# Optimization experiments

Measured on AMD Instinct MI355X. Metric: run time of the kernel, lower is better.

## Reference

```python
import jax, jax.numpy as jnp
import numpy as np

B, S, D, H, DFF = 65536, 9, 20, 4, 512
DH = D // H  # 5
EPS = 1e-5


def _layernorm(x, g, b):
    m = jnp.mean(x, axis=-1, keepdims=True)
    v = jnp.mean(jnp.square(x - m), axis=-1, keepdims=True)
    return (x - m) * jax.lax.rsqrt(v + EPS) * g + b


def setup_inputs() -> dict:
    key = jax.random.key(0)
    ks = jax.random.split(key, 8)
    s = 1.0 / np.sqrt(D)
    inp = {
        "inputs": jax.random.normal(ks[0], (B, S, D), dtype=jnp.float32),
        "Wq": jax.random.uniform(ks[1], (D, D), jnp.float32, -s, s),
        "bq": jnp.zeros((D,), jnp.float32),
        "Wk": jax.random.uniform(ks[2], (D, D), jnp.float32, -s, s),
        "bk": jnp.zeros((D,), jnp.float32),
        "Wv": jax.random.uniform(ks[3], (D, D), jnp.float32, -s, s),
        "bv": jnp.zeros((D,), jnp.float32),
        "Wo": jax.random.uniform(ks[4], (D, D), jnp.float32, -s, s),
        "bo": jnp.zeros((D,), jnp.float32),
        "g1": jnp.ones((D,), jnp.float32),
        "b1": jnp.zeros((D,), jnp.float32),
        "W1": jax.random.uniform(ks[5], (D, DFF), jnp.float32, -s, s),
        "W2": jax.random.uniform(ks[6], (DFF, D), jnp.float32, -1.0 / np.sqrt(DFF), 1.0 / np.sqrt(DFF)),
        "g2": jnp.ones((D,), jnp.float32),
        "b2": jnp.zeros((D,), jnp.float32),
    }
    return inp


def reference(inputs, Wq, bq, Wk, bk, Wv, bv, Wo, bo, g1, b1, W1, W2, g2, b2):
    x = inputs  # [B,S,D]
    q = (x @ Wq + bq).reshape(B, S, H, DH).transpose(0, 2, 1, 3)  # [B,H,S,dh]
    k = (x @ Wk + bk).reshape(B, S, H, DH).transpose(0, 2, 1, 3)
    v = (x @ Wv + bv).reshape(B, S, H, DH).transpose(0, 2, 1, 3)
    a = jnp.einsum('bhqd,bhkd->bhqk', q, k) / 3.0  # hardcoded /3 in source
    attn = jax.nn.softmax(a, axis=-1)
    ctx = jnp.einsum('bhqk,bhkd->bhqd', attn, v)  # [B,H,S,dh]
    # faithful quirk: transpose(2,3) then reshape to [B,9,20]
    merged = ctx.transpose(0, 1, 3, 2).reshape(B, S, D)
    attn_out = merged @ Wo + bo
    y = _layernorm(attn_out + x, g1, b1)
    ff = jax.nn.relu(y @ W1) @ W2
    return _layernorm(y + ff, g2, b2)
```

## Files before the change

kernel.cpp:

```cpp
#include <hip/hip_runtime.h>
#include <hip/hip_bf16.h>
#include <hip/hip_fp16.h>

#define B_TOT 65536
#define S 9
#define D 20
#define DFF 512
#define EPS 1e-5f

typedef short bf16x8 __attribute__((ext_vector_type(8)));
typedef _Float16 f16x8 __attribute__((ext_vector_type(8)));
typedef float f32x4 __attribute__((ext_vector_type(4)));

#define SH_PQKV 0
#define SH_PWOA 2560
#define FL_BQKV2 1792
#define FL_BO4 1872
#define SH_PA1 3872
#define SH_PB2 20256
#define PREP_TOTAL (2560 + 1024 + 144 + 16384 + 16384)

__device__ __forceinline__ unsigned short f2bf(float f) {
  union { __hip_bfloat16 h; unsigned short u; } v;
  v.h = __float2bfloat16(f);
  return v.u;
}
__device__ __forceinline__ unsigned short f2h(float f) {
  union { _Float16 h; unsigned short u; } v;
  v.h = (_Float16)f;
  return v.u;
}
__device__ __forceinline__ float bf2f(unsigned short h) {
  union { unsigned u; float f; } v; v.u = ((unsigned)h) << 16; return v.f;
}
__device__ __forceinline__ unsigned cvt2(float a, float b) {
  union { __hip_bfloat162 h; unsigned u; } v;
  v.h = __float22bfloat162_rn(make_float2(a, b));
  return v.u;
}
__device__ __forceinline__ unsigned cvt2h(float a, float b) {
  union { __half2 h; unsigned u; } v;
  v.h = __float22half2_rn(make_float2(a, b));
  return v.u;
}
__device__ __forceinline__ void unpk(unsigned u, float& lo, float& hi) {
  union { unsigned v; float f; } a, b;
  a.v = u << 16; b.v = u & 0xffff0000u;
  lo = a.f; hi = b.f;
}
__device__ __forceinline__ void unpack20_u2(const char* p, float* o) {
  uint2 r0 = *(const uint2*)p, r1 = *(const uint2*)(p + 8), r2 = *(const uint2*)(p + 16);
  uint2 r3 = *(const uint2*)(p + 24), r4 = *(const uint2*)(p + 32);
  unpk(r0.x, o[0], o[1]); unpk(r0.y, o[2], o[3]);
  unpk(r1.x, o[4], o[5]); unpk(r1.y, o[6], o[7]);
  unpk(r2.x, o[8], o[9]); unpk(r2.y, o[10], o[11]);
  unpk(r3.x, o[12], o[13]); unpk(r3.y, o[14], o[15]);
  unpk(r4.x, o[16], o[17]); unpk(r4.y, o[18], o[19]);
}

union h2u { unsigned u; __half2 h; };

__global__ void prep_kernel(const float* __restrict__ Wq, const float* __restrict__ Wk,
                            const float* __restrict__ Wv, const float* __restrict__ Wo,
                            const float* __restrict__ W1, const float* __restrict__ W2,
                            const float* __restrict__ bq, const float* __restrict__ bk,
                            const float* __restrict__ bv, const float* __restrict__ bo,
                            float* __restrict__ wsf) {
  int stride = gridDim.x * blockDim.x;
  unsigned short* P = (unsigned short*)wsf;
  for (int i = blockIdx.x * blockDim.x + threadIdx.x; i < PREP_TOTAL; i += stride) {
    if (i < 2560) {
      int ct = i >> 9, rem = i & 511, l = rem >> 3, jj = rem & 7;
      int g = l >> 4, cl = l & 15;
      int jp = ct * 16 + cl, d = 8 * g + jj;
      unsigned short v = 0;
      if (d < 20 && jp < 72) {
        int mat = jp / 24, r24 = jp % 24;
        int h = r24 / 6, c6 = r24 % 6;
        if (c6 < 5) {
          const float* Wsrc = (mat == 0) ? Wq : (mat == 1) ? Wk : Wv;
          v = f2bf(Wsrc[d * 20 + 5 * h + c6]);
        }
      }
      P[SH_PQKV + i] = v;
    } else if (i < 3584) {
      int p = i - 2560;
      int ct = p >> 9, rem = p & 511, l = rem >> 3, jj = rem & 7;
      int g = l >> 4, cl = l & 15;
      int j = ct * 16 + cl, d = 8 * g + jj;
      P[SH_PWOA + p] = (d < 20 && j < 20) ? f2bf(Wo[d * 20 + j]) : (unsigned short)0;
    } else if (i < 3728) {
      int j = i - 3584;
      if (j < 80) {
        float v = 0.f;
        if (j < 72) {
          int mat = j / 24, r24 = j % 24;
          int h = r24 / 6, c6 = r24 % 6;
          if (c6 < 5) {
            const float* bsrc = (mat == 0) ? bq : (mat == 1) ? bk : bv;
            v = bsrc[5 * h + c6];
          }
        }
        wsf[FL_BQKV2 + j] = v;
      } else {
        int jb = j - 80;
        wsf[FL_BO4 + jb] = (jb < 20) ? bo[jb] : 0.f;
      }
    } else if (i < 3728 + 16384) {
      int j = i - 3728;
      int frag = j >> 9, rem = j & 511;
      int l = rem >> 3, jj = rem & 7;
      int p = frag & 1, q2 = (frag >> 1) & 3, ch = frag >> 3;
      int g2 = l >> 4, cl2 = l & 15;
      int k = 8 * g2 + jj;
      int f = ch * 128 + q2 * 32 + 8 * (cl2 >> 2) + 4 * p + (cl2 & 3);
      P[SH_PA1 + j] = (k < 20) ? f2bf(W1[k * DFF + f]) : (unsigned short)0;
    } else {
      int j = i - (3728 + 16384);
      int pair = j >> 9, rem = j & 511;
      int l = rem >> 3, jj = rem & 7;
      int g = l >> 4, cl = l & 15;
      int kk = pair >> 1, cc = pair & 1;
      int kg = kk * 32 + 8 * g + jj;
      int d = cc * 16 + cl;
      P[SH_PB2 + j] = (d < 20) ? f2h(W2[kg * 20 + d]) : (unsigned short)0;
    }
  }
}

#define SLAB_BYTES 13312
#define RA 0
#define RB 7168

#define FENCE() asm volatile("" ::: "memory")

__global__ __launch_bounds__(256, 2) void encoder_kernel(
    const float* __restrict__ X, const float* __restrict__ ws,
    const float* __restrict__ g1, const float* __restrict__ b1,
    const float* __restrict__ g2, const float* __restrict__ b2,
    float* __restrict__ Out) {
  __shared__ __align__(16) char smem[4 * SLAB_BYTES];

  const unsigned short* P16 = (const unsigned short*)ws;
  const unsigned short* PQKV = P16 + SH_PQKV;
  const unsigned short* PWOA = P16 + SH_PWOA;
  const float* BQKV2 = ws + FL_BQKV2;
  const float* BO4 = ws + FL_BO4;
  const unsigned short* PA1 = P16 + SH_PA1;
  const unsigned short* PB2 = P16 + SH_PB2;

  const int tid = threadIdx.x;
  const int wv = tid >> 6;
  const int lane = tid & 63;
  const int bl = lane / 9;
  const int s = lane - bl * 9;
  const long wb = (long)blockIdx.x * 4 + wv;
  const long bb = wb * 7 + bl;
  const bool active = (bl < 7) && (bb < B_TOT);

  char* slab = smem + wv * SLAB_BYTES;
  const int cl = lane & 15;
  const int g = lane >> 4;
  const f32x4 zero4 = {0.f, 0.f, 0.f, 0.f};

  float x[20];

  {
    if (active) {
      const float4* xr = (const float4*)(X + bb * (S * D) + s * D);
#pragma unroll
      for (int i = 0; i < 5; ++i) {
        float4 t = xr[i];
        x[4 * i + 0] = t.x; x[4 * i + 1] = t.y; x[4 * i + 2] = t.z; x[4 * i + 3] = t.w;
      }
    } else {
#pragma unroll
      for (int i = 0; i < 20; ++i) x[i] = 0.f;
    }
    unsigned u[10];
#pragma unroll
    for (int i = 0; i < 10; ++i) u[i] = cvt2(x[2 * i], x[2 * i + 1]);
    uint4* dst = (uint4*)(slab + RA + lane * 112);
    dst[0] = make_uint4(u[0], u[1], u[2], u[3]);
    dst[1] = make_uint4(u[4], u[5], u[6], u[7]);
    dst[2] = make_uint4(u[8], u[9], 0u, 0u);
    dst[3] = make_uint4(0u, 0u, 0u, 0u);
  }
  FENCE();

  bf16x8 xfB[4];
#pragma unroll
  for (int rtc = 0; rtc < 4; ++rtc)
    xfB[rtc] = *(const bf16x8*)(slab + RA + (rtc * 16 + cl) * 112 + g * 16);
  FENCE();

#pragma unroll
  for (int ct = 0; ct < 5; ++ct) {
    bf16x8 wf = *(const bf16x8*)(PQKV + (size_t)(ct * 64 + lane) * 8);
    float4 bq4 = *(const float4*)(BQKV2 + ct * 16 + 4 * g);
    const f32x4 cin = {bq4.x, bq4.y, bq4.z, bq4.w};
    const int qd = ct * 4 + g;
    const int mat = (qd >= 12) ? 2 : ((qd >= 6) ? 1 : 0);
    const int jq = qd - 6 * mat;
    const bool qv = qd < 18;
#pragma unroll
    for (int rtc = 0; rtc < 4; ++rtc) {
      f32x4 d = __builtin_amdgcn_mfma_f32_16x16x32_bf16(wf, xfB[rtc], cin, 0, 0, 0);
      if (qv) {
        const int row = rtc * 16 + cl;
        unsigned u0 = cvt2h(d[0], d[1]);
        unsigned u1 = cvt2h(d[2], d[3]);
        char* p = (mat == 0) ? (slab + RA + row * 112 + 64 + jq * 8)
                             : (slab + RB + row * 96 + ((mat == 2) ? 48 : 0) + jq * 8);
        *(uint2*)p = make_uint2(u0, u1);
      }
    }
  }
  FENCE();

  float ctx[20];
  if (active) {
    h2u q2[12];
    {
      const uint2* qp = (const uint2*)(slab + RA + lane * 112 + 64);
#pragma unroll
      for (int i = 0; i < 6; ++i) { uint2 t = qp[i]; q2[2 * i].u = t.x; q2[2 * i + 1].u = t.y; }
    }
    float sc[4][9];
#pragma unroll
    for (int t = 0; t < 9; ++t) {
      h2u k2[12];
      const uint2* kp = (const uint2*)(slab + RB + (bl * 9 + t) * 96);
#pragma unroll
      for (int i = 0; i < 6; ++i) { uint2 tt = kp[i]; k2[2 * i].u = tt.x; k2[2 * i + 1].u = tt.y; }
#pragma unroll
      for (int h = 0; h < 4; ++h) {
        __half2 a = __hmul2(q2[3 * h].h, k2[3 * h].h);
        a = __hfma2(q2[3 * h + 1].h, k2[3 * h + 1].h, a);
        a = __hfma2(q2[3 * h + 2].h, k2[3 * h + 2].h, a);
        sc[h][t] = __low2float(a) + __high2float(a);
      }
    }
    float inv4[4];
#pragma unroll
    for (int h = 0; h < 4; ++h) {
      float mx = sc[h][0];
#pragma unroll
      for (int t = 1; t < 9; ++t) mx = fmaxf(mx, sc[h][t]);
      float sum = 0.f;
#pragma unroll
      for (int t = 0; t < 9; ++t) {
        sc[h][t] = __expf((sc[h][t] - mx) * (1.0f / 3.0f));
        sum += sc[h][t];
      }
      inv4[h] = 1.0f / sum;
    }
    h2u ctx2[12];
#pragma unroll
    for (int i = 0; i < 12; ++i) ctx2[i].u = 0u;
#pragma unroll
    for (int t = 0; t < 9; ++t) {
      h2u v2[12];
      const uint2* vp = (const uint2*)(slab + RB + (bl * 9 + t) * 96 + 48);
#pragma unroll
      for (int i = 0; i < 6; ++i) { uint2 tt = vp[i]; v2[2 * i].u = tt.x; v2[2 * i + 1].u = tt.y; }
#pragma unroll
      for (int h = 0; h < 4; ++h) {
        __half2 p2 = __float2half2_rn(sc[h][t]);
#pragma unroll
        for (int p3 = 0; p3 < 3; ++p3)
          ctx2[3 * h + p3].h = __hfma2(p2, v2[3 * h + p3].h, ctx2[3 * h + p3].h);
      }
    }
#pragma unroll
    for (int h = 0; h < 4; ++h) {
      ctx[5 * h + 0] = __low2float(ctx2[3 * h + 0].h) * inv4[h];
      ctx[5 * h + 1] = __high2float(ctx2[3 * h + 0].h) * inv4[h];
      ctx[5 * h + 2] = __low2float(ctx2[3 * h + 1].h) * inv4[h];
      ctx[5 * h + 3] = __high2float(ctx2[3 * h + 1].h) * inv4[h];
      ctx[5 * h + 4] = __low2float(ctx2[3 * h + 2].h) * inv4[h];
    }
  }
  FENCE();

  if (active) {
    int m = s;
#pragma unroll
    for (int w = 0; w < 20; ++w) {
      int row = (m * 3277) >> 16;
      int col = m - 20 * row;
      *(unsigned short*)(slab + RB + (bl * 9 + row) * 80 + col * 2) = f2bf(ctx[w]);
      m += 9;
    }
  } else {
    *(uint4*)(slab + RB + lane * 80) = make_uint4(0u, 0u, 0u, 0u);
    *(uint4*)(slab + RB + lane * 80 + 16) = make_uint4(0u, 0u, 0u, 0u);
    *(uint2*)(slab + RB + lane * 80 + 32) = make_uint2(0u, 0u);
  }
  *(uint2*)(slab + RB + lane * 80 + 40) = make_uint2(0u, 0u);
  *(uint4*)(slab + RB + lane * 80 + 48) = make_uint4(0u, 0u, 0u, 0u);
  FENCE();

  bf16x8 mfB[4];
#pragma unroll
  for (int rtc = 0; rtc < 4; ++rtc)
    mfB[rtc] = *(const bf16x8*)(slab + RB + (rtc * 16 + cl) * 80 + g * 16);
  FENCE();
#pragma unroll
  for (int ct = 0; ct < 2; ++ct) {
    bf16x8 wof = *(const bf16x8*)(PWOA + (size_t)(ct * 64 + lane) * 8);
    float4 bo4 = *(const float4*)(BO4 + ct * 16 + 4 * g);
    const f32x4 cin = {bo4.x, bo4.y, bo4.z, bo4.w};
    const int qd = ct * 4 + g;
    const bool qv = qd < 5;
#pragma unroll
    for (int rtc = 0; rtc < 4; ++rtc) {
      f32x4 d = __builtin_amdgcn_mfma_f32_16x16x32_bf16(wof, mfB[rtc], cin, 0, 0, 0);
      if (qv) {
        const int row = rtc * 16 + cl;
        *(float4*)(slab + RB + row * 80 + qd * 16) = make_float4(d[0], d[1], d[2], d[3]);
      }
    }
  }
  FENCE();

  float y[20];
  if (active) {
    float ao[20];
    {
      const float4* ap = (const float4*)(slab + RB + lane * 80);
#pragma unroll
      for (int i = 0; i < 5; ++i) {
        float4 t = ap[i];
        ao[4 * i] = t.x; ao[4 * i + 1] = t.y; ao[4 * i + 2] = t.z; ao[4 * i + 3] = t.w;
      }
    }
    float z[20];
#pragma unroll
    for (int d = 0; d < 20; ++d) z[d] = ao[d] + x[d];
    float t0 = 0.f;
#pragma unroll
    for (int d = 0; d < 20; ++d) t0 += z[d];
    float mean = t0 * (1.0f / 20.0f);
    float var = 0.f;
#pragma unroll
    for (int d = 0; d < 20; ++d) { z[d] -= mean; var += z[d] * z[d]; }
    float rs = rsqrtf(var * (1.0f / 20.0f) + EPS);
#pragma unroll
    for (int d = 0; d < 20; ++d) y[d] = z[d] * rs * g1[d] + b1[d];
  } else {
#pragma unroll
    for (int d = 0; d < 20; ++d) y[d] = 0.f;
  }
  FENCE();

  {
    unsigned u[10];
#pragma unroll
    for (int i = 0; i < 10; ++i) u[i] = cvt2(y[2 * i], y[2 * i + 1]);
    uint4* dst = (uint4*)(slab + RA + lane * 112);
    dst[0] = make_uint4(u[0], u[1], u[2], u[3]);
    dst[1] = make_uint4(u[4], u[5], u[6], u[7]);
    *(uint2*)(slab + RA + lane * 112 + 32) = make_uint2(u[8], u[9]);
  }
  FENCE();

  bf16x8 ytf[4];
#pragma unroll
  for (int rt = 0; rt < 4; ++rt)
    ytf[rt] = *(const bf16x8*)(slab + RA + (rt * 16 + cl) * 112 + g * 16);

  f32x4 acc[4][2];
#pragma unroll
  for (int rt = 0; rt < 4; ++rt) { acc[rt][0] = zero4; acc[rt][1] = zero4; }

  for (int ch = 0; ch < 4; ++ch) {
#pragma unroll
    for (int q2 = 0; q2 < 4; ++q2) {
      const int fb = ch * 8 + q2 * 2;
      bf16x8 aw0 = *(const bf16x8*)(PA1 + (size_t)(fb * 64 + lane) * 8);
      bf16x8 aw1 = *(const bf16x8*)(PA1 + (size_t)((fb + 1) * 64 + lane) * 8);
      f16x8 bw0 = *(const f16x8*)(PB2 + (size_t)(fb * 64 + lane) * 8);
      f16x8 bw1 = *(const f16x8*)(PB2 + (size_t)((fb + 1) * 64 + lane) * 8);
#pragma unroll
      for (int rt = 0; rt < 4; ++rt) {
        f32x4 d0 = __builtin_amdgcn_mfma_f32_16x16x32_bf16(aw0, ytf[rt], zero4, 0, 0, 0);
        f32x4 d1 = __builtin_amdgcn_mfma_f32_16x16x32_bf16(aw1, ytf[rt], zero4, 0, 0, 0);
        union { f16x8 v; unsigned uu[4]; } af;
        af.uu[0] = cvt2h(fmaxf(d0[0], 0.f), fmaxf(d0[1], 0.f));
        af.uu[1] = cvt2h(fmaxf(d0[2], 0.f), fmaxf(d0[3], 0.f));
        af.uu[2] = cvt2h(fmaxf(d1[0], 0.f), fmaxf(d1[1], 0.f));
        af.uu[3] = cvt2h(fmaxf(d1[2], 0.f), fmaxf(d1[3], 0.f));
        acc[rt][0] = __builtin_amdgcn_mfma_f32_16x16x32_f16(af.v, bw0, acc[rt][0], 0, 0, 0);
        acc[rt][1] = __builtin_amdgcn_mfma_f32_16x16x32_f16(af.v, bw1, acc[rt][1], 0, 0, 0);
      }
    }
  }

#pragma unroll
  for (int rt = 0; rt < 4; ++rt) {
#pragma unroll
    for (int r = 0; r < 4; ++r) {
      const int rrow = rt * 16 + 4 * g + r;
      *(float*)(slab + RB + rrow * 88 + cl * 4) = acc[rt][0][r];
      if (cl < 4) *(float*)(slab + RB + rrow * 88 + 64 + cl * 4) = acc[rt][1][r];
    }
  }
  FENCE();

  if (active) {
    float z[20];
    {
      const char* fp = slab + RB + lane * 88;
#pragma unroll
      for (int i = 0; i < 10; ++i) {
        float2 t = *(const float2*)(fp + 8 * i);
        z[2 * i] = t.x; z[2 * i + 1] = t.y;
      }
    }
    float yr[20];
    unpack20_u2(slab + RA + lane * 112, yr);
    float t0 = 0.f;
#pragma unroll
    for (int d = 0; d < 20; ++d) { z[d] += yr[d]; t0 += z[d]; }
    float mean = t0 * (1.0f / 20.0f);
    float var = 0.f;
#pragma unroll
    for (int d = 0; d < 20; ++d) { z[d] -= mean; var += z[d] * z[d]; }
    float rs = rsqrtf(var * (1.0f / 20.0f) + EPS);
    float o[20];
#pragma unroll
    for (int d = 0; d < 20; ++d) o[d] = z[d] * rs * g2[d] + b2[d];
    float4* op = (float4*)(Out + (wb * 63 + lane) * 20);
#pragma unroll
    for (int i = 0; i < 5; ++i)
      op[i] = make_float4(o[4 * i], o[4 * i + 1], o[4 * i + 2], o[4 * i + 3]);
  }
}

extern "C" void kernel_launch(void* const* d_in, const int* in_sizes, int n_in,
                              void* d_out, int out_size, void* d_ws, size_t ws_size,
                              hipStream_t stream) {
  const float* X  = (const float*)d_in[0];
  const float* Wq = (const float*)d_in[1];
  const float* bq = (const float*)d_in[2];
  const float* Wk = (const float*)d_in[3];
  const float* bk = (const float*)d_in[4];
  const float* Wv = (const float*)d_in[5];
  const float* bv = (const float*)d_in[6];
  const float* Wo = (const float*)d_in[7];
  const float* bo = (const float*)d_in[8];
  const float* g1 = (const float*)d_in[9];
  const float* b1 = (const float*)d_in[10];
  const float* W1 = (const float*)d_in[11];
  const float* W2 = (const float*)d_in[12];
  const float* g2 = (const float*)d_in[13];
  const float* b2 = (const float*)d_in[14];
  float* Out = (float*)d_out;
  float* ws = (float*)d_ws;

  prep_kernel<<<144, 256, 0, stream>>>(Wq, Wk, Wv, Wo, W1, W2, bq, bk, bv, bo, ws);

  int nblocks = (B_TOT + 27) / 28;
  encoder_kernel<<<nblocks, 256, 0, stream>>>(X, ws, g1, b1, g2, b2, Out);
}
```

Baseline: 85.27 us.

## Pack QKV projection densely, shrink LDS slabs, and use packed f16 ReLU

```diff
diff --git a/kernel.cpp b/kernel.cpp
--- a/kernel.cpp
+++ b/kernel.cpp
@@ -13,12 +13,12 @@
 typedef float f32x4 __attribute__((ext_vector_type(4)));
 
 #define SH_PQKV 0
-#define SH_PWOA 2560
-#define FL_BQKV2 1792
-#define FL_BO4 1872
-#define SH_PA1 3872
-#define SH_PB2 20256
-#define PREP_TOTAL (2560 + 1024 + 144 + 16384 + 16384)
+#define SH_PWOA 2048
+#define FL_BQKV 1536
+#define FL_BO4 1600
+#define SH_PA1 3328
+#define SH_PB2 19712
+#define PREP_TOTAL (2048 + 1024 + 128 + 16384 + 16384)
 
 __device__ __forceinline__ unsigned short f2bf(float f) {
   union { __hip_bfloat16 h; unsigned short u; } v;
@@ -30,9 +30,6 @@
   v.h = (_Float16)f;
   return v.u;
 }
-__device__ __forceinline__ float bf2f(unsigned short h) {
-  union { unsigned u; float f; } v; v.u = ((unsigned)h) << 16; return v.f;
-}
 __device__ __forceinline__ unsigned cvt2(float a, float b) {
   union { __hip_bfloat162 h; unsigned u; } v;
   v.h = __float22bfloat162_rn(make_float2(a, b));
@@ -43,19 +40,10 @@
   v.h = __float22half2_rn(make_float2(a, b));
   return v.u;
 }
-__device__ __forceinline__ void unpk(unsigned u, float& lo, float& hi) {
-  union { unsigned v; float f; } a, b;
-  a.v = u << 16; b.v = u & 0xffff0000u;
-  lo = a.f; hi = b.f;
-}
-__device__ __forceinline__ void unpack20_u2(const char* p, float* o) {
-  uint2 r0 = *(const uint2*)p, r1 = *(const uint2*)(p + 8), r2 = *(const uint2*)(p + 16);
-  uint2 r3 = *(const uint2*)(p + 24), r4 = *(const uint2*)(p + 32);
-  unpk(r0.x, o[0], o[1]); unpk(r0.y, o[2], o[3]);
-  unpk(r1.x, o[4], o[5]); unpk(r1.y, o[6], o[7]);
-  unpk(r2.x, o[8], o[9]); unpk(r2.y, o[10], o[11]);
-  unpk(r3.x, o[12], o[13]); unpk(r3.y, o[14], o[15]);
-  unpk(r4.x, o[16], o[17]); unpk(r4.y, o[18], o[19]);
+__device__ __forceinline__ unsigned pkmax0(unsigned a, unsigned z) {
+  unsigned r;
+  asm("v_pk_max_f16 %0, %1, %2" : "=v"(r) : "v"(a), "v"(z));
+  return r;
 }
 
 union h2u { unsigned u; __half2 h; };
@@ -69,45 +57,33 @@
   int stride = gridDim.x * blockDim.x;
   unsigned short* P = (unsigned short*)wsf;
   for (int i = blockIdx.x * blockDim.x + threadIdx.x; i < PREP_TOTAL; i += stride) {
-    if (i < 2560) {
+    if (i < 2048) {
       int ct = i >> 9, rem = i & 511, l = rem >> 3, jj = rem & 7;
       int g = l >> 4, cl = l & 15;
-      int jp = ct * 16 + cl, d = 8 * g + jj;
+      int j = ct * 16 + cl, d = 8 * g + jj;
       unsigned short v = 0;
-      if (d < 20 && jp < 72) {
-        int mat = jp / 24, r24 = jp % 24;
-        int h = r24 / 6, c6 = r24 % 6;
-        if (c6 < 5) {
-          const float* Wsrc = (mat == 0) ? Wq : (mat == 1) ? Wk : Wv;
-          v = f2bf(Wsrc[d * 20 + 5 * h + c6]);
-        }
+      if (d < 20 && j < 60) {
+        int mat = j / 20, jc = j % 20;
+        const float* Wsrc = (mat == 0) ? Wq : (mat == 1) ? Wk : Wv;
+        v = f2bf(Wsrc[d * 20 + jc]);
       }
       P[SH_PQKV + i] = v;
-    } else if (i < 3584) {
-      int p = i - 2560;
+    } else if (i < 3072) {
+      int p = i - 2048;
       int ct = p >> 9, rem = p & 511, l = rem >> 3, jj = rem & 7;
       int g = l >> 4, cl = l & 15;
       int j = ct * 16 + cl, d = 8 * g + jj;
       P[SH_PWOA + p] = (d < 20 && j < 20) ? f2bf(Wo[d * 20 + j]) : (unsigned short)0;
-    } else if (i < 3728) {
-      int j = i - 3584;
-      if (j < 80) {
-        float v = 0.f;
-        if (j < 72) {
-          int mat = j / 24, r24 = j % 24;
-          int h = r24 / 6, c6 = r24 % 6;
-          if (c6 < 5) {
-            const float* bsrc = (mat == 0) ? bq : (mat == 1) ? bk : bv;
-            v = bsrc[5 * h + c6];
-          }
-        }
-        wsf[FL_BQKV2 + j] = v;
-      } else {
-        int jb = j - 80;
-        wsf[FL_BO4 + jb] = (jb < 20) ? bo[jb] : 0.f;
-      }
-    } else if (i < 3728 + 16384) {
-      int j = i - 3728;
+    } else if (i < 3200) {
+      int j = i - 3072;
+      float v = 0.f;
+      if (j < 20) v = bq[j];
+      else if (j < 40) v = bk[j - 20];
+      else if (j < 60) v = bv[j - 40];
+      else if (j >= 64 && j < 84) v = bo[j - 64];
+      wsf[FL_BQKV + j] = v;
+    } else if (i < 3200 + 16384) {
+      int j = i - 3200;
       int frag = j >> 9, rem = j & 511;
       int l = rem >> 3, jj = rem & 7;
       int p = frag & 1, q2 = (frag >> 1) & 3, ch = frag >> 3;
@@ -116,7 +92,7 @@
       int f = ch * 128 + q2 * 32 + 8 * (cl2 >> 2) + 4 * p + (cl2 & 3);
       P[SH_PA1 + j] = (k < 20) ? f2bf(W1[k * DFF + f]) : (unsigned short)0;
     } else {
-      int j = i - (3728 + 16384);
+      int j = i - (3200 + 16384);
       int pair = j >> 9, rem = j & 511;
       int l = rem >> 3, jj = rem & 7;
       int g = l >> 4, cl = l & 15;
@@ -128,9 +104,9 @@
   }
 }
 
-#define SLAB_BYTES 13312
+#define SLAB_BYTES 9728
 #define RA 0
-#define RB 7168
+#define RB 4608
 
 #define FENCE() asm volatile("" ::: "memory")
 
@@ -144,7 +120,7 @@
   const unsigned short* P16 = (const unsigned short*)ws;
   const unsigned short* PQKV = P16 + SH_PQKV;
   const unsigned short* PWOA = P16 + SH_PWOA;
-  const float* BQKV2 = ws + FL_BQKV2;
+  const float* BQKV = ws + FL_BQKV;
   const float* BO4 = ws + FL_BO4;
   const unsigned short* PA1 = P16 + SH_PA1;
   const unsigned short* PB2 = P16 + SH_PB2;
@@ -177,32 +153,32 @@
 #pragma unroll
       for (int i = 0; i < 20; ++i) x[i] = 0.f;
     }
-    unsigned u[10];
-#pragma unroll
-    for (int i = 0; i < 10; ++i) u[i] = cvt2(x[2 * i], x[2 * i + 1]);
-    uint4* dst = (uint4*)(slab + RA + lane * 112);
-    dst[0] = make_uint4(u[0], u[1], u[2], u[3]);
-    dst[1] = make_uint4(u[4], u[5], u[6], u[7]);
-    dst[2] = make_uint4(u[8], u[9], 0u, 0u);
-    dst[3] = make_uint4(0u, 0u, 0u, 0u);
+    char* r = slab + RA + lane * 72;
+#pragma unroll
+    for (int i = 0; i < 5; ++i)
+      *(uint2*)(r + 8 * i) = make_uint2(cvt2(x[4 * i], x[4 * i + 1]),
+                                        cvt2(x[4 * i + 2], x[4 * i + 3]));
+    *(uint2*)(r + 40) = make_uint2(0u, 0u);
+    *(uint2*)(r + 48) = make_uint2(0u, 0u);
+    *(uint2*)(r + 56) = make_uint2(0u, 0u);
   }
   FENCE();
 
   bf16x8 xfB[4];
 #pragma unroll
   for (int rtc = 0; rtc < 4; ++rtc)
-    xfB[rtc] = *(const bf16x8*)(slab + RA + (rtc * 16 + cl) * 112 + g * 16);
-  FENCE();
-
-#pragma unroll
-  for (int ct = 0; ct < 5; ++ct) {
+    xfB[rtc] = *(const bf16x8*)(slab + RA + (rtc * 16 + cl) * 72 + g * 16);
+  FENCE();
+
+#pragma unroll
+  for (int ct = 0; ct < 4; ++ct) {
     bf16x8 wf = *(const bf16x8*)(PQKV + (size_t)(ct * 64 + lane) * 8);
-    float4 bq4 = *(const float4*)(BQKV2 + ct * 16 + 4 * g);
+    float4 bq4 = *(const float4*)(BQKV + ct * 16 + 4 * g);
     const f32x4 cin = {bq4.x, bq4.y, bq4.z, bq4.w};
     const int qd = ct * 4 + g;
-    const int mat = (qd >= 12) ? 2 : ((qd >= 6) ? 1 : 0);
-    const int jq = qd - 6 * mat;
-    const bool qv = qd < 18;
+    const int mat = (qd >= 10) ? 2 : ((qd >= 5) ? 1 : 0);
+    const int jc4 = qd - 5 * mat;
+    const bool qv = qd < 15;
 #pragma unroll
     for (int rtc = 0; rtc < 4; ++rtc) {
       f32x4 d = __builtin_amdgcn_mfma_f32_16x16x32_bf16(wf, xfB[rtc], cin, 0, 0, 0);
@@ -210,8 +186,8 @@
         const int row = rtc * 16 + cl;
         unsigned u0 = cvt2h(d[0], d[1]);
         unsigned u1 = cvt2h(d[2], d[3]);
-        char* p = (mat == 0) ? (slab + RA + row * 112 + 64 + jq * 8)
-                             : (slab + RB + row * 96 + ((mat == 2) ? 48 : 0) + jq * 8);
+        char* p = (mat == 0) ? (slab + RA + row * 72 + jc4 * 8)
+                             : (slab + RB + row * 80 + ((mat == 2) ? 40 : 0) + jc4 * 8);
         *(uint2*)p = make_uint2(u0, u1);
       }
     }
@@ -220,26 +196,35 @@
 
   float ctx[20];
   if (active) {
-    h2u q2[12];
+    h2u q2[10];
     {
-      const uint2* qp = (const uint2*)(slab + RA + lane * 112 + 64);
-#pragma unroll
-      for (int i = 0; i < 6; ++i) { uint2 t = qp[i]; q2[2 * i].u = t.x; q2[2 * i + 1].u = t.y; }
+      const uint2* qp = (const uint2*)(slab + RA + lane * 72);
+#pragma unroll
+      for (int i = 0; i < 5; ++i) { uint2 t = qp[i]; q2[2 * i].u = t.x; q2[2 * i + 1].u = t.y; }
     }
     float sc[4][9];
 #pragma unroll
     for (int t = 0; t < 9; ++t) {
-      h2u k2[12];
-      const uint2* kp = (const uint2*)(slab + RB + (bl * 9 + t) * 96);
-#pragma unroll
-      for (int i = 0; i < 6; ++i) { uint2 tt = kp[i]; k2[2 * i].u = tt.x; k2[2 * i + 1].u = tt.y; }
-#pragma unroll
-      for (int h = 0; h < 4; ++h) {
-        __half2 a = __hmul2(q2[3 * h].h, k2[3 * h].h);
-        a = __hfma2(q2[3 * h + 1].h, k2[3 * h + 1].h, a);
-        a = __hfma2(q2[3 * h + 2].h, k2[3 * h + 2].h, a);
-        sc[h][t] = __low2float(a) + __high2float(a);
-      }
+      h2u k2[10];
+      const char* kp = slab + RB + (bl * 9 + t) * 80;
+      {
+        uint4 a = *(const uint4*)kp;
+        uint4 b = *(const uint4*)(kp + 16);
+        uint2 c = *(const uint2*)(kp + 32);
+        k2[0].u = a.x; k2[1].u = a.y; k2[2].u = a.z; k2[3].u = a.w;
+        k2[4].u = b.x; k2[5].u = b.y; k2[6].u = b.z; k2[7].u = b.w;
+        k2[8].u = c.x; k2[9].u = c.y;
+      }
+      __half2 a0 = __hmul2(q2[0].h, k2[0].h); a0 = __hfma2(q2[1].h, k2[1].h, a0);
+      __half2 m2 = __hmul2(q2[2].h, k2[2].h);
+      __half2 a1 = __hmul2(q2[3].h, k2[3].h); a1 = __hfma2(q2[4].h, k2[4].h, a1);
+      __half2 a2 = __hmul2(q2[5].h, k2[5].h); a2 = __hfma2(q2[6].h, k2[6].h, a2);
+      __half2 m7 = __hmul2(q2[7].h, k2[7].h);
+      __half2 a3 = __hmul2(q2[8].h, k2[8].h); a3 = __hfma2(q2[9].h, k2[9].h, a3);
+      sc[0][t] = __low2float(a0) + __high2float(a0) + __low2float(m2);
+      sc[1][t] = __high2float(m2) + __low2float(a1) + __high2float(a1);
+      sc[2][t] = __low2float(a2) + __high2float(a2) + __low2float(m7);
+      sc[3][t] = __high2float(m7) + __low2float(a3) + __high2float(a3);
     }
     float inv4[4];
 #pragma unroll
@@ -255,30 +240,43 @@
       }
       inv4[h] = 1.0f / sum;
     }
-    h2u ctx2[12];
-#pragma unroll
-    for (int i = 0; i < 12; ++i) ctx2[i].u = 0u;
+    h2u ctx2[10];
+#pragma unroll
+    for (int i = 0; i < 10; ++i) ctx2[i].u = 0u;
 #pragma unroll
     for (int t = 0; t < 9; ++t) {
-      h2u v2[12];
-      const uint2* vp = (const uint2*)(slab + RB + (bl * 9 + t) * 96 + 48);
-#pragma unroll
-      for (int i = 0; i < 6; ++i) { uint2 tt = vp[i]; v2[2 * i].u = tt.x; v2[2 * i + 1].u = tt.y; }
-#pragma unroll
-      for (int h = 0; h < 4; ++h) {
-        __half2 p2 = __float2half2_rn(sc[h][t]);
-#pragma unroll
-        for (int p3 = 0; p3 < 3; ++p3)
-          ctx2[3 * h + p3].h = __hfma2(p2, v2[3 * h + p3].h, ctx2[3 * h + p3].h);
-      }
-    }
-#pragma unroll
-    for (int h = 0; h < 4; ++h) {
-      ctx[5 * h + 0] = __low2float(ctx2[3 * h + 0].h) * inv4[h];
-      ctx[5 * h + 1] = __high2float(ctx2[3 * h + 0].h) * inv4[h];
-      ctx[5 * h + 2] = __low2float(ctx2[3 * h + 1].h) * inv4[h];
-      ctx[5 * h + 3] = __high2float(ctx2[3 * h + 1].h) * inv4[h];
-      ctx[5 * h + 4] = __low2float(ctx2[3 * h + 2].h) * inv4[h];
+      h2u v2[10];
+      const char* vp = slab + RB + (bl * 9 + t) * 80 + 40;
+      {
+        uint2 a = *(const uint2*)vp;
+        uint4 b = *(const uint4*)(vp + 8);
+        uint4 c = *(const uint4*)(vp + 24);
+        v2[0].u = a.x; v2[1].u = a.y;
+        v2[2].u = b.x; v2[3].u = b.y; v2[4].u = b.z; v2[5].u = b.w;
+        v2[6].u = c.x; v2[7].u = c.y; v2[8].u = c.z; v2[9].u = c.w;
+      }
+      h2u p00, p11, p22, p33, m01, m23;
+      p00.h = __float2half2_rn(sc[0][t]);
+      p11.h = __float2half2_rn(sc[1][t]);
+      p22.h = __float2half2_rn(sc[2][t]);
+      p33.h = __float2half2_rn(sc[3][t]);
+      m01.u = cvt2h(sc[0][t], sc[1][t]);
+      m23.u = cvt2h(sc[2][t], sc[3][t]);
+      ctx2[0].h = __hfma2(p00.h, v2[0].h, ctx2[0].h);
+      ctx2[1].h = __hfma2(p00.h, v2[1].h, ctx2[1].h);
+      ctx2[2].h = __hfma2(m01.h, v2[2].h, ctx2[2].h);
+      ctx2[3].h = __hfma2(p11.h, v2[3].h, ctx2[3].h);
+      ctx2[4].h = __hfma2(p11.h, v2[4].h, ctx2[4].h);
+      ctx2[5].h = __hfma2(p22.h, v2[5].h, ctx2[5].h);
+      ctx2[6].h = __hfma2(p22.h, v2[6].h, ctx2[6].h);
+      ctx2[7].h = __hfma2(m23.h, v2[7].h, ctx2[7].h);
+      ctx2[8].h = __hfma2(p33.h, v2[8].h, ctx2[8].h);
+      ctx2[9].h = __hfma2(p33.h, v2[9].h, ctx2[9].h);
+    }
+#pragma unroll
+    for (int p = 0; p < 10; ++p) {
+      ctx[2 * p] = __low2float(ctx2[p].h) * inv4[(2 * p) / 5];
+      ctx[2 * p + 1] = __high2float(ctx2[p].h) * inv4[(2 * p + 1) / 5];
     }
   }
   FENCE();
@@ -355,25 +353,27 @@
   FENCE();
 
   {
-    unsigned u[10];
-#pragma unroll
-    for (int i = 0; i < 10; ++i) u[i] = cvt2(y[2 * i], y[2 * i + 1]);
-    uint4* dst = (uint4*)(slab + RA + lane * 112);
-    dst[0] = make_uint4(u[0], u[1], u[2], u[3]);
-    dst[1] = make_uint4(u[4], u[5], u[6], u[7]);
-    *(uint2*)(slab + RA + lane * 112 + 32) = make_uint2(u[8], u[9]);
+    char* r = slab + RA + lane * 72;
+#pragma unroll
+    for (int i = 0; i < 5; ++i)
+      *(uint2*)(r + 8 * i) = make_uint2(cvt2(y[4 * i], y[4 * i + 1]),
+                                        cvt2(y[4 * i + 2], y[4 * i + 3]));
+    *(uint2*)(r + 40) = make_uint2(0u, 0u);
+    *(uint2*)(r + 48) = make_uint2(0u, 0u);
+    *(uint2*)(r + 56) = make_uint2(0u, 0u);
   }
   FENCE();
 
   bf16x8 ytf[4];
 #pragma unroll
   for (int rt = 0; rt < 4; ++rt)
-    ytf[rt] = *(const bf16x8*)(slab + RA + (rt * 16 + cl) * 112 + g * 16);
+    ytf[rt] = *(const bf16x8*)(slab + RA + (rt * 16 + cl) * 72 + g * 16);
 
   f32x4 acc[4][2];
 #pragma unroll
   for (int rt = 0; rt < 4; ++rt) { acc[rt][0] = zero4; acc[rt][1] = zero4; }
 
+  const unsigned zz = 0u;
   for (int ch = 0; ch < 4; ++ch) {
 #pragma unroll
     for (int q2 = 0; q2 < 4; ++q2) {
@@ -387,10 +387,10 @@
         f32x4 d0 = __builtin_amdgcn_mfma_f32_16x16x32_bf16(aw0, ytf[rt], zero4, 0, 0, 0);
         f32x4 d1 = __builtin_amdgcn_mfma_f32_16x16x32_bf16(aw1, ytf[rt], zero4, 0, 0, 0);
         union { f16x8 v; unsigned uu[4]; } af;
-        af.uu[0] = cvt2h(fmaxf(d0[0], 0.f), fmaxf(d0[1], 0.f));
-        af.uu[1] = cvt2h(fmaxf(d0[2], 0.f), fmaxf(d0[3], 0.f));
-        af.uu[2] = cvt2h(fmaxf(d1[0], 0.f), fmaxf(d1[1], 0.f));
-        af.uu[3] = cvt2h(fmaxf(d1[2], 0.f), fmaxf(d1[3], 0.f));
+        af.uu[0] = pkmax0(cvt2h(d0[0], d0[1]), zz);
+        af.uu[1] = pkmax0(cvt2h(d0[2], d0[3]), zz);
+        af.uu[2] = pkmax0(cvt2h(d1[0], d1[1]), zz);
+        af.uu[3] = pkmax0(cvt2h(d1[2], d1[3]), zz);
         acc[rt][0] = __builtin_amdgcn_mfma_f32_16x16x32_f16(af.v, bw0, acc[rt][0], 0, 0, 0);
         acc[rt][1] = __builtin_amdgcn_mfma_f32_16x16x32_f16(af.v, bw1, acc[rt][1], 0, 0, 0);
       }
@@ -402,8 +402,8 @@
 #pragma unroll
     for (int r = 0; r < 4; ++r) {
       const int rrow = rt * 16 + 4 * g + r;
-      *(float*)(slab + RB + rrow * 88 + cl * 4) = acc[rt][0][r];
-      if (cl < 4) *(float*)(slab + RB + rrow * 88 + 64 + cl * 4) = acc[rt][1][r];
+      *(float*)(slab + RB + rrow * 80 + cl * 4) = acc[rt][0][r];
+      if (cl < 4) *(float*)(slab + RB + rrow * 80 + 64 + cl * 4) = acc[rt][1][r];
     }
   }
   FENCE();
@@ -411,18 +411,16 @@
   if (active) {
     float z[20];
     {
-      const char* fp = slab + RB + lane * 88;
-#pragma unroll
-      for (int i = 0; i < 10; ++i) {
-        float2 t = *(const float2*)(fp + 8 * i);
-        z[2 * i] = t.x; z[2 * i + 1] = t.y;
-      }
-    }
-    float yr[20];
-    unpack20_u2(slab + RA + lane * 112, yr);
+      const float4* fp = (const float4*)(slab + RB + lane * 80);
+#pragma unroll
+      for (int i = 0; i < 5; ++i) {
+        float4 t = fp[i];
+        z[4 * i] = t.x; z[4 * i + 1] = t.y; z[4 * i + 2] = t.z; z[4 * i + 3] = t.w;
+      }
+    }
     float t0 = 0.f;
 #pragma unroll
-    for (int d = 0; d < 20; ++d) { z[d] += yr[d]; t0 += z[d]; }
+    for (int d = 0; d < 20; ++d) { z[d] += y[d]; t0 += z[d]; }
     float mean = t0 * (1.0f / 20.0f);
     float var = 0.f;
 #pragma unroll
```

Result: faster. 71.89 us (-15.7%).
